# Optimization experiments

Measured on AMD Instinct MI355X. Metric: run time of the kernel, lower is better.

## Reference

```python
import jax, jax.numpy as jnp
import numpy as np

N_HEADS = 16
MAX_CACHE_LEN = 8192
LN_EPS = 1e-5


def _layernorm(x, g, b):
    mu = jnp.mean(x, axis=-1, keepdims=True)
    var = jnp.var(x, axis=-1, keepdims=True)
    return (x - mu) * jax.lax.rsqrt(var + LN_EPS) * g + b


def setup_inputs() -> dict:
    key = jax.random.key(0)
    ks = jax.random.split(key, 8)
    b, t, d, latdim, past = 2, 2048, 2048, 512, 2048
    s = 0.02
    return {
        "x": jax.random.normal(ks[0], (b, t, d), jnp.float32),
        "latent_prev": jax.random.normal(ks[1], (b, past, latdim), jnp.float32),
        "Wq": jax.random.normal(ks[2], (d, d), jnp.float32) * s,
        "Wdown": jax.random.normal(ks[3], (d, latdim), jnp.float32) * s,
        "Wk_up": jax.random.normal(ks[4], (latdim, d), jnp.float32) * s,
        "Wv_up": jax.random.normal(ks[5], (latdim, d), jnp.float32) * s,
        "ln_g": jnp.ones((latdim,), jnp.float32),
        "ln_b": jnp.zeros((latdim,), jnp.float32),
        "Wo": jax.random.normal(ks[6], (d, d), jnp.float32) * s,
    }


def reference(x, latent_prev, Wq, Wdown, Wk_up, Wv_up, ln_g, ln_b, Wo):
    b, t, d = x.shape
    H = N_HEADS
    hd = d // H
    # q projection -> [b, t, H, hd]
    q = (x @ Wq).reshape(b, t, H, hd)
    # latent down-projection + LayerNorm, concat with cache, trim to max_cache_len
    latent_new = _layernorm(x @ Wdown, ln_g, ln_b)
    latent = jnp.concatenate([latent_prev, latent_new], axis=1)
    latent = latent[:, -MAX_CACHE_LEN:]
    S = latent.shape[1]
    past_len = min(latent_prev.shape[1], S - t)
    # up-project K/V from latent -> [b, S, H, hd]
    k = (latent @ Wk_up).reshape(b, S, H, hd)
    v = (latent @ Wv_up).reshape(b, S, H, hd)
    # offset-causal SDPA: query i attends keys j <= past_len + i
    scores = jnp.einsum("bthd,bshd->bhts", q, k) / jnp.sqrt(jnp.asarray(hd, x.dtype))
    i = jnp.arange(t)[:, None]
    j = jnp.arange(S)[None, :]
    mask = j <= (past_len + i)  # [t, S]
    scores = jnp.where(mask[None, None], scores, jnp.asarray(-1e30, scores.dtype))
    attn = jax.nn.softmax(scores, axis=-1)
    out = jnp.einsum("bhts,bshd->bthd", attn, v).reshape(b, t, d)
    return out @ Wo
```

## Files before the change

### kernel.cpp

```cpp
#include <hip/hip_runtime.h>
#include <hip/hip_bf16.h>

using bf16_t = __bf16;
typedef __bf16 bf16x8 __attribute__((ext_vector_type(8)));
typedef __bf16 bf16x4 __attribute__((ext_vector_type(4)));
typedef __bf16 bf16x2 __attribute__((ext_vector_type(2)));
typedef float  f32x4  __attribute__((ext_vector_type(4)));
typedef float  f32x16 __attribute__((ext_vector_type(16)));
typedef unsigned u32x4 __attribute__((ext_vector_type(4)));

#define MFMA16(a,b,c) __builtin_amdgcn_mfma_f32_16x16x32_bf16((a),(b),(c),0,0,0)
#define MFMA32(a,b,c) __builtin_amdgcn_mfma_f32_32x32x16_bf16((a),(b),(c),0,0,0)

__device__ __forceinline__ void load_lds16(const void* g, void* l) {
  __builtin_amdgcn_global_load_lds(
      (const __attribute__((address_space(1))) unsigned int*)g,
      (__attribute__((address_space(3))) unsigned int*)l, 16, 0, 0);
}

__device__ __forceinline__ unsigned pack_bf16(float a, float b) {
  union { bf16x2 v; unsigned u; } c;
  c.v[0] = (bf16_t)a; c.v[1] = (bf16_t)b;
  return c.u;
}

__device__ __forceinline__ float fast_exp2(float x) {
#if __has_builtin(__builtin_amdgcn_exp2f)
  return __builtin_amdgcn_exp2f(x);
#else
  return exp2f(x);
#endif
}

__device__ __forceinline__ void xcd_remap(unsigned& bx, unsigned& by,
                                          unsigned& bz)
{
  const unsigned nxy = gridDim.x * gridDim.y;
  const unsigned nwg = nxy * gridDim.z;
  unsigned wg = (blockIdx.z * gridDim.y + blockIdx.y) * gridDim.x + blockIdx.x;
  if ((nwg & 7u) == 0u)
    wg = (wg & 7u) * (nwg >> 3) + (wg >> 3);
  bz = wg / nxy; wg -= bz * nxy;
  by = wg / gridDim.x;
  bx = wg - by * gridDim.x;
}

__device__ __forceinline__ void transpose_body(const float* __restrict__ in,
                                               bf16_t* __restrict__ out,
                                               int R, int C, int bx, int by,
                                               int tid, bf16_t* t)
{
  const int r0 = by * 64, c0 = bx * 64;
  const int rr = tid >> 4;
  const int c4 = (tid & 15) * 4;
#pragma unroll
  for (int i = 0; i < 4; ++i) {
    const int r = rr + i * 16;
    f32x4 d = *(const f32x4*)(in + (size_t)(r0 + r) * C + c0 + c4);
#pragma unroll
    for (int j = 0; j < 4; ++j) t[(c4 + j) * 80 + r] = (bf16_t)d[j];
  }
  __syncthreads();
  const int a  = tid >> 3;
  const int bc = (tid & 7) * 8;
#pragma unroll
  for (int half = 0; half < 2; ++half) {
    const int cc = a + half * 32;
    bf16x8 d = *(const bf16x8*)&t[cc * 80 + bc];
    *(bf16x8*)(out + (size_t)(c0 + cc) * R + r0 + bc) = d;
  }
}

__global__ __launch_bounds__(256) void prep_all(
    const float* __restrict__ x,     bf16_t* __restrict__ xb,
    const float* __restrict__ Wq,    bf16_t* __restrict__ WqT,
    const float* __restrict__ Wdown, bf16_t* __restrict__ WdT,
    const float* __restrict__ Wo,    bf16_t* __restrict__ WoT,
    const float* __restrict__ Wk,    bf16_t* __restrict__ WkT,
    const float* __restrict__ Wv,    bf16_t* __restrict__ WvT,
    const float* __restrict__ prev,  bf16_t* __restrict__ latent)
{
  __shared__ __align__(16) bf16_t t[64 * 80];
  const int tid = threadIdx.x;
  const unsigned bid = blockIdx.x;
  if (bid < 8192) {
    const size_t i = ((size_t)bid * 256 + tid) * 4;
    f32x4 d = *(const f32x4*)(x + i);
    bf16x4 o;
#pragma unroll
    for (int j = 0; j < 4; ++j) o[j] = (bf16_t)d[j];
    *(bf16x4*)(xb + i) = o;
  } else if (bid < 9216) {
    const unsigned u = bid - 8192;
    transpose_body(Wq, WqT, 2048, 2048, u & 31, u >> 5, tid, t);
  } else if (bid < 9472) {
    const unsigned u = bid - 9216;
    transpose_body(Wdown, WdT, 2048, 512, u & 7, u >> 3, tid, t);
  } else if (bid < 10496) {
    const unsigned u = bid - 9472;
    transpose_body(Wo, WoT, 2048, 2048, u & 31, u >> 5, tid, t);
  } else if (bid < 10752) {
    const unsigned u = bid - 10496;
    transpose_body(Wk, WkT, 512, 2048, u & 31, u >> 5, tid, t);
  } else if (bid < 11008) {
    const unsigned u = bid - 10752;
    transpose_body(Wv, WvT, 512, 2048, u & 31, u >> 5, tid, t);
  } else {
    const size_t v    = (size_t)(bid - 11008) * 256 + tid;
    const size_t flat = v * 4;
    const size_t per  = (size_t)2048 * 512;
    const size_t b    = flat / per, rem = flat % per;
    f32x4 d = *(const f32x4*)(prev + flat);
    bf16x4 o;
#pragma unroll
    for (int j = 0; j < 4; ++j) o[j] = (bf16_t)d[j];
    *(bf16x4*)(latent + b * ((size_t)4096 * 512) + rem) = o;
  }
}

template <typename OutT>
__global__ __launch_bounds__(256) void gemm128(const bf16_t* __restrict__ A,
                                               const bf16_t* __restrict__ BT,
                                               OutT* __restrict__ C,
                                               int M, int N, int K, float scale,
                                               long long zB, long long zC)
{
  __shared__ __align__(16) bf16_t As[128 * 64];
  __shared__ __align__(16) bf16_t Bs[128 * 64];
  const int tid = threadIdx.x;
  unsigned bx, by, bz;
  xcd_remap(bx, by, bz);
  BT += (size_t)bz * zB;
  C  += (size_t)bz * zC;
  const int m0 = by * 128, n0 = bx * 128;
  const int lane = tid & 63, w = tid >> 6;
  const int quad = lane >> 4, l15 = lane & 15;
  const int wm = (w >> 1) * 64, wn = (w & 1) * 64;
  const int s_row = tid >> 3;
  const int g_off = ((tid & 7) ^ (s_row & 7)) * 8;
  const bf16_t* Ap = A  + (size_t)(m0 + s_row) * K + g_off;
  const bf16_t* Bp = BT + (size_t)(n0 + s_row) * K + g_off;
  const int cpos0 = (quad ^ (l15 & 7)) * 8;
  const int cpos1 = ((4 + quad) ^ (l15 & 7)) * 8;

  f32x4 acc[4][4] = {};

  for (int k0 = 0; k0 < K; k0 += 64) {
    __syncthreads();
#pragma unroll
    for (int p = 0; p < 4; ++p) {
      load_lds16(Ap + (size_t)(32 * p) * K + k0, As + (tid + 256 * p) * 8);
      load_lds16(Bp + (size_t)(32 * p) * K + k0, Bs + (tid + 256 * p) * 8);
    }
    __syncthreads();
#pragma unroll
    for (int kk = 0; kk < 2; ++kk) {
      const int cp = kk ? cpos1 : cpos0;
      bf16x8 af[4], bfr[4];
#pragma unroll
      for (int fi = 0; fi < 4; ++fi)
        af[fi] = *(const bf16x8*)&As[(wm + fi * 16 + l15) * 64 + cp];
#pragma unroll
      for (int fj = 0; fj < 4; ++fj)
        bfr[fj] = *(const bf16x8*)&Bs[(wn + fj * 16 + l15) * 64 + cp];
#pragma unroll
      for (int fi = 0; fi < 4; ++fi)
#pragma unroll
        for (int fj = 0; fj < 4; ++fj)
          acc[fi][fj] = MFMA16(af[fi], bfr[fj], acc[fi][fj]);
    }
  }

#pragma unroll
  for (int fi = 0; fi < 4; ++fi)
#pragma unroll
    for (int fj = 0; fj < 4; ++fj)
#pragma unroll
      for (int r = 0; r < 4; ++r) {
        const int row = m0 + wm + fi * 16 + quad * 4 + r;
        const int col = n0 + wn + fj * 16 + l15;
        C[(size_t)row * N + col] = (OutT)(acc[fi][fj][r] * scale);
      }
}

__global__ __launch_bounds__(256) void gemm128_dual(const bf16_t* __restrict__ A,
                                                    const bf16_t* __restrict__ BT,
                                                    bf16_t* __restrict__ C1,
                                                    bf16_t* __restrict__ C2,
                                                    float qscale)
{
  __shared__ __align__(16) bf16_t As[128 * 64];
  __shared__ __align__(16) bf16_t Bs[128 * 64];
  const int tid = threadIdx.x;
  unsigned bx, by, bz;
  xcd_remap(bx, by, bz);
  const int K = 2048;
  const int m0 = by * 128, n0 = bx * 128;
  const int lane = tid & 63, w = tid >> 6;
  const int quad = lane >> 4, l15 = lane & 15;
  const int wm = (w >> 1) * 64, wn = (w & 1) * 64;
  const int s_row = tid >> 3;
  const int g_off = ((tid & 7) ^ (s_row & 7)) * 8;
  const bf16_t* Ap = A  + (size_t)(m0 + s_row) * K + g_off;
  const bf16_t* Bp = BT + (size_t)(n0 + s_row) * K + g_off;
  const int cpos0 = (quad ^ (l15 & 7)) * 8;
  const int cpos1 = ((4 + quad) ^ (l15 & 7)) * 8;

  f32x4 acc[4][4] = {};

  for (int k0 = 0; k0 < K; k0 += 64) {
    __syncthreads();
#pragma unroll
    for (int p = 0; p < 4; ++p) {
      load_lds16(Ap + (size_t)(32 * p) * K + k0, As + (tid + 256 * p) * 8);
      load_lds16(Bp + (size_t)(32 * p) * K + k0, Bs + (tid + 256 * p) * 8);
    }
    __syncthreads();
#pragma unroll
    for (int kk = 0; kk < 2; ++kk) {
      const int cp = kk ? cpos1 : cpos0;
      bf16x8 af[4], bfr[4];
#pragma unroll
      for (int fi = 0; fi < 4; ++fi)
        af[fi] = *(const bf16x8*)&As[(wm + fi * 16 + l15) * 64 + cp];
#pragma unroll
      for (int fj = 0; fj < 4; ++fj)
        bfr[fj] = *(const bf16x8*)&Bs[(wn + fj * 16 + l15) * 64 + cp];
#pragma unroll
      for (int fi = 0; fi < 4; ++fi)
#pragma unroll
        for (int fj = 0; fj < 4; ++fj)
          acc[fi][fj] = MFMA16(af[fi], bfr[fj], acc[fi][fj]);
    }
  }

  const bool isQ = (n0 < 2048);
  const float sc = isQ ? qscale : 1.0f;
#pragma unroll
  for (int fi = 0; fi < 4; ++fi)
#pragma unroll
    for (int fj = 0; fj < 4; ++fj)
#pragma unroll
      for (int r = 0; r < 4; ++r) {
        const int row = m0 + wm + fi * 16 + quad * 4 + r;
        const int col = n0 + wn + fj * 16 + l15;
        if (isQ)
          C1[(size_t)row * 2048 + col] = (bf16_t)(acc[fi][fj][r] * sc);
        else
          C2[(size_t)row * 512 + (col - 2048)] = (bf16_t)(acc[fi][fj][r] * sc);
      }
}

__global__ __launch_bounds__(256) void gemm_kv(const bf16_t* __restrict__ latent,
                                               const bf16_t* __restrict__ WkT,
                                               const bf16_t* __restrict__ WvT,
                                               bf16_t* __restrict__ kbuf,
                                               bf16_t* __restrict__ vTb)
{
  __shared__ __align__(16) bf16_t As[128 * 64];
  __shared__ __align__(16) bf16_t Bs[128 * 64];
  const int tid = threadIdx.x;
  unsigned wg = blockIdx.x;
  wg = (wg & 7u) * 256u + (wg >> 3);
  const bf16_t *A, *BT;
  bf16_t* C;
  int M, N;
  unsigned bx, by;
  if (wg < 1024) {
    bx = wg & 15; by = wg >> 4;
    A = latent; BT = WkT; C = kbuf; M = 8192; N = 2048;
  } else {
    const unsigned t2 = wg - 1024;
    const unsigned bz = t2 >> 9, rem = t2 & 511;
    bx = rem & 31; by = rem >> 5;
    A  = WvT;
    BT = latent + (size_t)bz * ((size_t)4096 * 512);
    C  = vTb + (size_t)bz * ((size_t)2048 * 4096);
    M = 2048; N = 4096;
  }
  const int K = 512;
  const int m0 = by * 128, n0 = bx * 128;
  const int lane = tid & 63, w = tid >> 6;
  const int quad = lane >> 4, l15 = lane & 15;
  const int wm = (w >> 1) * 64, wn = (w & 1) * 64;
  const int s_row = tid >> 3;
  const int g_off = ((tid & 7) ^ (s_row & 7)) * 8;
  const bf16_t* Ap = A  + (size_t)(m0 + s_row) * K + g_off;
  const bf16_t* Bp = BT + (size_t)(n0 + s_row) * K + g_off;
  const int cpos0 = (quad ^ (l15 & 7)) * 8;
  const int cpos1 = ((4 + quad) ^ (l15 & 7)) * 8;

  f32x4 acc[4][4] = {};

  for (int k0 = 0; k0 < K; k0 += 64) {
    __syncthreads();
#pragma unroll
    for (int p = 0; p < 4; ++p) {
      load_lds16(Ap + (size_t)(32 * p) * K + k0, As + (tid + 256 * p) * 8);
      load_lds16(Bp + (size_t)(32 * p) * K + k0, Bs + (tid + 256 * p) * 8);
    }
    __syncthreads();
#pragma unroll
    for (int kk = 0; kk < 2; ++kk) {
      const int cp = kk ? cpos1 : cpos0;
      bf16x8 af[4], bfr[4];
#pragma unroll
      for (int fi = 0; fi < 4; ++fi)
        af[fi] = *(const bf16x8*)&As[(wm + fi * 16 + l15) * 64 + cp];
#pragma unroll
      for (int fj = 0; fj < 4; ++fj)
        bfr[fj] = *(const bf16x8*)&Bs[(wn + fj * 16 + l15) * 64 + cp];
#pragma unroll
      for (int fi = 0; fi < 4; ++fi)
#pragma unroll
        for (int fj = 0; fj < 4; ++fj)
          acc[fi][fj] = MFMA16(af[fi], bfr[fj], acc[fi][fj]);
    }
  }

#pragma unroll
  for (int fi = 0; fi < 4; ++fi)
#pragma unroll
    for (int fj = 0; fj < 4; ++fj)
#pragma unroll
      for (int r = 0; r < 4; ++r) {
        const int row = m0 + wm + fi * 16 + quad * 4 + r;
        const int col = n0 + wn + fj * 16 + l15;
        C[(size_t)row * N + col] = (bf16_t)acc[fi][fj][r];
      }
}

__global__ __launch_bounds__(256) void ln_kernel(const bf16_t* __restrict__ in,
                                                 const float* __restrict__ g_,
                                                 const float* __restrict__ b_,
                                                 bf16_t* __restrict__ latent)
{
  const int row = blockIdx.x;
  const int tid = threadIdx.x;
  const float x0 = (float)in[(size_t)row * 512 + tid];
  const float x1 = (float)in[(size_t)row * 512 + 256 + tid];
  float s  = x0 + x1;
  float sq = x0 * x0 + x1 * x1;
#pragma unroll
  for (int off = 1; off < 64; off <<= 1) {
    s  += __shfl_xor(s, off);
    sq += __shfl_xor(sq, off);
  }
  __shared__ float red[8];
  const int w = tid >> 6;
  if ((tid & 63) == 0) { red[w] = s; red[4 + w] = sq; }
  __syncthreads();
  s  = red[0] + red[1] + red[2] + red[3];
  sq = red[4] + red[5] + red[6] + red[7];
  const float mu   = s * (1.0f / 512.0f);
  const float var  = sq * (1.0f / 512.0f) - mu * mu;
  const float rstd = rsqrtf(var + 1e-5f);
  const int b = row >> 11, tt = row & 2047;
  bf16_t* outp = latent + ((size_t)b * 4096 + 2048 + tt) * 512;
  outp[tid]       = (bf16_t)((x0 - mu) * rstd * g_[tid]       + b_[tid]);
  outp[tid + 256] = (bf16_t)((x1 - mu) * rstd * g_[tid + 256] + b_[tid + 256]);
}

__global__ __launch_bounds__(256) void attn7(const bf16_t* __restrict__ q,
                                             const bf16_t* __restrict__ k,
                                             const bf16_t* __restrict__ vT,
                                             bf16_t* __restrict__ out)
{
  __shared__ __align__(16) bf16_t smem[32768];

  const int tid = threadIdx.x;
  const int lane = tid & 63, w = tid >> 6;
  const int l31 = lane & 31, h5 = lane >> 5;

  const int g = blockIdx.x & 7, j = blockIdx.x >> 3;
  const int jl = j & 31, hsel = j >> 5;
  int qt = jl & 15;
  const int b = jl >> 4;
  if (hsel) qt = 15 - qt;
  const int h = g + 8 * hsel;

  const int q0 = qt * 128;
  const int qg = q0 + l31 * 4 + w;

  bf16x8 qf[8];
  const bf16_t* qb = q + ((size_t)(b * 2048 + qg)) * 2048 + h * 128 + h5 * 8;
#pragma unroll
  for (int fc = 0; fc < 8; ++fc) qf[fc] = *(const bf16x8*)(qb + fc * 16);

  const bf16_t* kbase = k + ((size_t)b * 4096) * 2048 + h * 128;
  const bf16_t* vbase = vT + ((size_t)(b * 16 + h)) * 128 * 4096;

  int ks_key[4], ks_go[4], vs_feat[4], vs_go[4];
#pragma unroll
  for (int p = 0; p < 4; ++p) {
    const int slot = tid + 256 * p;
    const int key = slot >> 4, ph = slot & 15;
    ks_key[p] = key;
    ks_go[p]  = (((ph & 8) | ((ph & 7) ^ (key & 7)))) * 8;
    const int ft = slot >> 3, p2 = slot & 7;
    vs_feat[p] = ft;
    vs_go[p]   = (p2 ^ (ft & 7)) * 8;
  }
  int kfo[8], vfo[4];
#pragma unroll
  for (int fc = 0; fc < 8; ++fc) {
    const int L = fc * 2 + h5;
    kfo[fc] = l31 * 128 + ((L & 8) | ((L & 7) ^ (l31 & 7))) * 8;
  }
#pragma unroll
  for (int kc = 0; kc < 4; ++kc) {
    const int L = kc * 2 + h5;
    vfo[kc] = l31 * 64 + (L ^ (l31 & 7)) * 8;
  }

  f32x16 o[4] = {};
  float m = -1e30f, l = 0.f;
  const int send = 2048 + q0 + 128;

#pragma unroll
  for (int p = 0; p < 4; ++p) {
    load_lds16(kbase + (size_t)ks_key[p] * 2048 + ks_go[p],
               smem + (tid + 256 * p) * 8);
    load_lds16(vbase + (size_t)vs_feat[p] * 4096 + vs_go[p],
               smem + 16384 + (tid + 256 * p) * 8);
  }
  __syncthreads();

  int cur = 0;
  for (int s0 = 0; s0 < send; s0 += 64) {
    const int s1 = s0 + 64;
    if (s1 < send) {
      const int nxt = (cur ^ 1) * 8192;
#pragma unroll
      for (int p = 0; p < 4; ++p) {
        load_lds16(kbase + (size_t)(s1 + ks_key[p]) * 2048 + ks_go[p],
                   smem + nxt + (tid + 256 * p) * 8);
        load_lds16(vbase + (size_t)vs_feat[p] * 4096 + s1 + vs_go[p],
                   smem + 16384 + nxt + (tid + 256 * p) * 8);
      }
    }
    const bf16_t* Kc = smem + cur * 8192;
    const bf16_t* Vc = smem + 16384 + cur * 8192;

    f32x16 st[2] = {};
    __builtin_amdgcn_s_setprio(1);
#pragma unroll
    for (int fc = 0; fc < 8; ++fc) {
      bf16x8 k0 = *(const bf16x8*)&Kc[kfo[fc]];
      bf16x8 k1 = *(const bf16x8*)&Kc[4096 + kfo[fc]];
      st[0] = MFMA32(k0, qf[fc], st[0]);
      st[1] = MFMA32(k1, qf[fc], st[1]);
    }
    __builtin_amdgcn_s_setprio(0);

    if (s0 + 63 > 2048 + q0) {
#pragma unroll
      for (int t = 0; t < 2; ++t)
#pragma unroll
        for (int i = 0; i < 16; ++i) {
          const int key = s0 + 32 * t + (i & 3) + 8 * (i >> 2) + 4 * h5;
          if (key > 2048 + qg) st[t][i] = -1e30f;
        }
    }

    float gm[8];
#pragma unroll
    for (int t = 0; t < 2; ++t)
#pragma unroll
      for (int gg = 0; gg < 4; ++gg)
        gm[t * 4 + gg] = fmaxf(fmaxf(st[t][4 * gg + 0], st[t][4 * gg + 1]),
                               fmaxf(st[t][4 * gg + 2], st[t][4 * gg + 3]));
    float mt = fmaxf(fmaxf(fmaxf(gm[0], gm[1]), fmaxf(gm[2], gm[3])),
                     fmaxf(fmaxf(gm[4], gm[5]), fmaxf(gm[6], gm[7])));
    mt = fmaxf(mt, __shfl_xor(mt, 32));

    if (__any(mt > m + 8.f)) {
      const float mnew = fmaxf(m, mt);
      const float alpha = fast_exp2(m - mnew);
#pragma unroll
      for (int ft = 0; ft < 4; ++ft)
#pragma unroll
        for (int i = 0; i < 16; ++i) o[ft][i] *= alpha;
      l *= alpha;
      m = mnew;
    }

    float rs = 0.f;
    unsigned up[2][4][2];
#pragma unroll
    for (int t = 0; t < 2; ++t)
#pragma unroll
      for (int gg = 0; gg < 4; ++gg) {
        const float p0 = fast_exp2(st[t][4 * gg + 0] - m);
        const float p1 = fast_exp2(st[t][4 * gg + 1] - m);
        const float p2 = fast_exp2(st[t][4 * gg + 2] - m);
        const float p3 = fast_exp2(st[t][4 * gg + 3] - m);
        rs += (p0 + p1) + (p2 + p3);
        up[t][gg][0] = pack_bf16(p0, p1);
        up[t][gg][1] = pack_bf16(p2, p3);
      }
    rs += __shfl_xor(rs, 32);
    l += rs;

#pragma unroll
    for (int kc = 0; kc < 4; ++kc) {
      const int t = kc >> 1, gp = (kc & 1) * 2;
      const unsigned a0 = up[t][gp][0],     a1 = up[t][gp][1];
      const unsigned b0 = up[t][gp + 1][0], b1 = up[t][gp + 1][1];
      const unsigned xa0 = __shfl_xor(a0, 32), xa1 = __shfl_xor(a1, 32);
      const unsigned xb0 = __shfl_xor(b0, 32), xb1 = __shfl_xor(b1, 32);
      u32x4 uw;
      uw[0] = h5 ? xb0 : a0;
      uw[1] = h5 ? xb1 : a1;
      uw[2] = h5 ? b0 : xa0;
      uw[3] = h5 ? b1 : xa1;
      union { u32x4 u; bf16x8 v; } pc; pc.u = uw;
      const bf16x8 pf = pc.v;
      __builtin_amdgcn_s_setprio(1);
#pragma unroll
      for (int ft = 0; ft < 4; ++ft) {
        bf16x8 vf = *(const bf16x8*)&Vc[ft * 2048 + vfo[kc]];
        o[ft] = MFMA32(vf, pf, o[ft]);
      }
      __builtin_amdgcn_s_setprio(0);
    }

    __syncthreads();
    cur ^= 1;
  }

  const float inv = 1.0f / l;
  const int rowp_w = w * 32 + l31;
#pragma unroll
  for (int ft = 0; ft < 4; ++ft)
#pragma unroll
    for (int gg = 0; gg < 4; ++gg) {
      bf16x4 pk;
#pragma unroll
      for (int r = 0; r < 4; ++r) pk[r] = (bf16_t)(o[ft][4 * gg + r] * inv);
      *(bf16x4*)&smem[rowp_w * 136 + ft * 32 + gg * 8 + h5 * 4] = pk;
    }
  __syncthreads();
#pragma unroll
  for (int p = 0; p < 8; ++p) {
    const int c = tid + 256 * p;
    const int rowp = c >> 4, chk = c & 15;
    const int ql = (rowp & 31) * 4 + (rowp >> 5);
    bf16x8 d = *(const bf16x8*)&smem[rowp * 136 + chk * 8];
    *(bf16x8*)(out + ((size_t)(b * 2048 + q0 + ql)) * 2048 + h * 128 + chk * 8) = d;
  }
}

extern "C" void kernel_launch(void* const* d_in, const int* in_sizes, int n_in,
                              void* d_out, int out_size, void* d_ws, size_t ws_size,
                              hipStream_t stream)
{
  (void)in_sizes; (void)n_in; (void)out_size; (void)ws_size;
  const float* x        = (const float*)d_in[0];
  const float* lat_prev = (const float*)d_in[1];
  const float* Wq       = (const float*)d_in[2];
  const float* Wdown    = (const float*)d_in[3];
  const float* Wk_up    = (const float*)d_in[4];
  const float* Wv_up    = (const float*)d_in[5];
  const float* ln_g     = (const float*)d_in[6];
  const float* ln_b     = (const float*)d_in[7];
  const float* Wo       = (const float*)d_in[8];
  float* out = (float*)d_out;

  char* p = (char*)d_ws;
  auto alloc = [&](size_t elems) { bf16_t* r = (bf16_t*)p; p += elems * 2; return r; };
  bf16_t* xb     = alloc((size_t)4096 * 2048);
  bf16_t* WqT    = alloc((size_t)2048 * 2048);
  bf16_t* WdT    = alloc((size_t)512 * 2048);
  bf16_t* qbuf   = alloc((size_t)4096 * 2048);
  bf16_t* latpre = alloc((size_t)4096 * 512);
  bf16_t* latent = alloc((size_t)2 * 4096 * 512);
  bf16_t* kbuf   = alloc((size_t)8192 * 2048);
  bf16_t* vTb    = alloc((size_t)2 * 2048 * 4096);
  bf16_t* aout   = alloc((size_t)4096 * 2048);
  bf16_t* WoT    = alloc((size_t)2048 * 2048);
  bf16_t* WkT    = alloc((size_t)2048 * 512);
  bf16_t* WvT    = alloc((size_t)2048 * 512);

  const dim3 B(256);
  const float qscale = 0.12751744561825988f;

  prep_all<<<dim3(13056), B, 0, stream>>>(x, xb, Wq, WqT, Wdown, WdT,
                                          Wo, WoT, Wk_up, WkT, Wv_up, WvT,
                                          lat_prev, latent);
  gemm128_dual<<<dim3(20, 32), B, 0, stream>>>(xb, WqT, qbuf, latpre, qscale);
  ln_kernel<<<dim3(4096), B, 0, stream>>>(latpre, ln_g, ln_b, latent);
  gemm_kv<<<dim3(2048), B, 0, stream>>>(latent, WkT, WvT, kbuf, vTb);
  attn7<<<dim3(512), B, 0, stream>>>(qbuf, kbuf, vTb, aout);
  gemm128<float><<<dim3(16, 32), B, 0, stream>>>(aout, WoT, out, 4096, 2048, 2048, 1.0f, 0, 0);
}
```

Baseline: 506.8 us.

## Double-buffer LDS in GEMM kernels with 32-wide K tiles

Replaces the single-buffer 64-wide K loop in the three GEMM kernels with a two-stage LDS ping-pong over 32-wide K tiles. The next tile is prefetched with global_load_lds while MFMAs run on the current one, and the swizzle is adapted to 4 chunks per row. This is meant to hide global load latency and remove one barrier per iteration. In exchange each iteration does half the MFMA work, so barrier count per unit of K stays the same. There is also a risk of a race, because the async LDS loads into the other buffer may not be waited on before the single barrier.

Result: no change. 501.8 us (-1.0%).

```diff
diff --git a/kernel.cpp b/kernel.cpp
--- a/kernel.cpp
+++ b/kernel.cpp
@@ -118,6 +118,39 @@
   }
 }
 
+#define GEMM_DBUF_LOOP(Kvar)                                                  \
+  f32x4 acc[4][4] = {};                                                       \
+  auto stage = [&](int k0, int buf) {                                         \
+    bf16_t* Ad = As + buf * 4096;                                             \
+    bf16_t* Bd = Bs + buf * 4096;                                             \
+    load_lds16(Ap0 + k0, Ad + tid * 8);                                       \
+    load_lds16(Ap1 + k0, Ad + tid * 8 + 2048);                                \
+    load_lds16(Bp0 + k0, Bd + tid * 8);                                       \
+    load_lds16(Bp1 + k0, Bd + tid * 8 + 2048);                                \
+  };                                                                          \
+  stage(0, 0);                                                                \
+  __syncthreads();                                                            \
+  int cur = 0;                                                                \
+  for (int k0 = 0; k0 < (Kvar); k0 += 32) {                                   \
+    if (k0 + 32 < (Kvar)) stage(k0 + 32, cur ^ 1);                            \
+    const bf16_t* Ac = As + cur * 4096;                                       \
+    const bf16_t* Bc = Bs + cur * 4096;                                       \
+    bf16x8 af[4], bfr[4];                                                     \
+    _Pragma("unroll")                                                         \
+    for (int fi = 0; fi < 4; ++fi)                                            \
+      af[fi] = *(const bf16x8*)&Ac[(wm + fi * 16 + l15) * 32 + quadp];        \
+    _Pragma("unroll")                                                         \
+    for (int fj = 0; fj < 4; ++fj)                                            \
+      bfr[fj] = *(const bf16x8*)&Bc[(wn + fj * 16 + l15) * 32 + quadp];       \
+    _Pragma("unroll")                                                         \
+    for (int fi = 0; fi < 4; ++fi)                                            \
+      _Pragma("unroll")                                                       \
+      for (int fj = 0; fj < 4; ++fj)                                          \
+        acc[fi][fj] = MFMA16(af[fi], bfr[fj], acc[fi][fj]);                   \
+    __syncthreads();                                                          \
+    cur ^= 1;                                                                 \
+  }
+
 template <typename OutT>
 __global__ __launch_bounds__(256) void gemm128(const bf16_t* __restrict__ A,
                                                const bf16_t* __restrict__ BT,
@@ -125,8 +158,8 @@
                                                int M, int N, int K, float scale,
                                                long long zB, long long zC)
 {
-  __shared__ __align__(16) bf16_t As[128 * 64];
-  __shared__ __align__(16) bf16_t Bs[128 * 64];
+  __shared__ __align__(16) bf16_t As[2 * 128 * 32];
+  __shared__ __align__(16) bf16_t Bs[2 * 128 * 32];
   const int tid = threadIdx.x;
   unsigned bx, by, bz;
   xcd_remap(bx, by, bz);
@@ -136,40 +169,15 @@
   const int lane = tid & 63, w = tid >> 6;
   const int quad = lane >> 4, l15 = lane & 15;
   const int wm = (w >> 1) * 64, wn = (w & 1) * 64;
-  const int s_row = tid >> 3;
-  const int g_off = ((tid & 7) ^ (s_row & 7)) * 8;
-  const bf16_t* Ap = A  + (size_t)(m0 + s_row) * K + g_off;
-  const bf16_t* Bp = BT + (size_t)(n0 + s_row) * K + g_off;
-  const int cpos0 = (quad ^ (l15 & 7)) * 8;
-  const int cpos1 = ((4 + quad) ^ (l15 & 7)) * 8;
-
-  f32x4 acc[4][4] = {};
-
-  for (int k0 = 0; k0 < K; k0 += 64) {
-    __syncthreads();
-#pragma unroll
-    for (int p = 0; p < 4; ++p) {
-      load_lds16(Ap + (size_t)(32 * p) * K + k0, As + (tid + 256 * p) * 8);
-      load_lds16(Bp + (size_t)(32 * p) * K + k0, Bs + (tid + 256 * p) * 8);
-    }
-    __syncthreads();
-#pragma unroll
-    for (int kk = 0; kk < 2; ++kk) {
-      const int cp = kk ? cpos1 : cpos0;
-      bf16x8 af[4], bfr[4];
-#pragma unroll
-      for (int fi = 0; fi < 4; ++fi)
-        af[fi] = *(const bf16x8*)&As[(wm + fi * 16 + l15) * 64 + cp];
-#pragma unroll
-      for (int fj = 0; fj < 4; ++fj)
-        bfr[fj] = *(const bf16x8*)&Bs[(wn + fj * 16 + l15) * 64 + cp];
-#pragma unroll
-      for (int fi = 0; fi < 4; ++fi)
-#pragma unroll
-        for (int fj = 0; fj < 4; ++fj)
-          acc[fi][fj] = MFMA16(af[fi], bfr[fj], acc[fi][fj]);
-    }
-  }
+  const int s_row = tid >> 2;
+  const int g_off = ((tid & 3) ^ (s_row & 3)) * 8;
+  const int quadp = (quad ^ (l15 & 3)) * 8;
+  const bf16_t* Ap0 = A  + (size_t)(m0 + s_row) * K + g_off;
+  const bf16_t* Ap1 = A  + (size_t)(m0 + 64 + s_row) * K + g_off;
+  const bf16_t* Bp0 = BT + (size_t)(n0 + s_row) * K + g_off;
+  const bf16_t* Bp1 = BT + (size_t)(n0 + 64 + s_row) * K + g_off;
+
+  GEMM_DBUF_LOOP(K)
 
 #pragma unroll
   for (int fi = 0; fi < 4; ++fi)
@@ -189,8 +197,8 @@
                                                     bf16_t* __restrict__ C2,
                                                     float qscale)
 {
-  __shared__ __align__(16) bf16_t As[128 * 64];
-  __shared__ __align__(16) bf16_t Bs[128 * 64];
+  __shared__ __align__(16) bf16_t As[2 * 128 * 32];
+  __shared__ __align__(16) bf16_t Bs[2 * 128 * 32];
   const int tid = threadIdx.x;
   unsigned bx, by, bz;
   xcd_remap(bx, by, bz);
@@ -199,40 +207,15 @@
   const int lane = tid & 63, w = tid >> 6;
   const int quad = lane >> 4, l15 = lane & 15;
   const int wm = (w >> 1) * 64, wn = (w & 1) * 64;
-  const int s_row = tid >> 3;
-  const int g_off = ((tid & 7) ^ (s_row & 7)) * 8;
-  const bf16_t* Ap = A  + (size_t)(m0 + s_row) * K + g_off;
-  const bf16_t* Bp = BT + (size_t)(n0 + s_row) * K + g_off;
-  const int cpos0 = (quad ^ (l15 & 7)) * 8;
-  const int cpos1 = ((4 + quad) ^ (l15 & 7)) * 8;
-
-  f32x4 acc[4][4] = {};
-
-  for (int k0 = 0; k0 < K; k0 += 64) {
-    __syncthreads();
-#pragma unroll
-    for (int p = 0; p < 4; ++p) {
-      load_lds16(Ap + (size_t)(32 * p) * K + k0, As + (tid + 256 * p) * 8);
-      load_lds16(Bp + (size_t)(32 * p) * K + k0, Bs + (tid + 256 * p) * 8);
-    }
-    __syncthreads();
-#pragma unroll
-    for (int kk = 0; kk < 2; ++kk) {
-      const int cp = kk ? cpos1 : cpos0;
-      bf16x8 af[4], bfr[4];
-#pragma unroll
-      for (int fi = 0; fi < 4; ++fi)
-        af[fi] = *(const bf16x8*)&As[(wm + fi * 16 + l15) * 64 + cp];
-#pragma unroll
-      for (int fj = 0; fj < 4; ++fj)
-        bfr[fj] = *(const bf16x8*)&Bs[(wn + fj * 16 + l15) * 64 + cp];
-#pragma unroll
-      for (int fi = 0; fi < 4; ++fi)
-#pragma unroll
-        for (int fj = 0; fj < 4; ++fj)
-          acc[fi][fj] = MFMA16(af[fi], bfr[fj], acc[fi][fj]);
-    }
-  }
+  const int s_row = tid >> 2;
+  const int g_off = ((tid & 3) ^ (s_row & 3)) * 8;
+  const int quadp = (quad ^ (l15 & 3)) * 8;
+  const bf16_t* Ap0 = A  + (size_t)(m0 + s_row) * K + g_off;
+  const bf16_t* Ap1 = A  + (size_t)(m0 + 64 + s_row) * K + g_off;
+  const bf16_t* Bp0 = BT + (size_t)(n0 + s_row) * K + g_off;
+  const bf16_t* Bp1 = BT + (size_t)(n0 + 64 + s_row) * K + g_off;
+
+  GEMM_DBUF_LOOP(K)
 
   const bool isQ = (n0 < 2048);
   const float sc = isQ ? qscale : 1.0f;
@@ -257,18 +240,18 @@
                                                bf16_t* __restrict__ kbuf,
                                                bf16_t* __restrict__ vTb)
 {
-  __shared__ __align__(16) bf16_t As[128 * 64];
-  __shared__ __align__(16) bf16_t Bs[128 * 64];
+  __shared__ __align__(16) bf16_t As[2 * 128 * 32];
+  __shared__ __align__(16) bf16_t Bs[2 * 128 * 32];
   const int tid = threadIdx.x;
   unsigned wg = blockIdx.x;
   wg = (wg & 7u) * 256u + (wg >> 3);
   const bf16_t *A, *BT;
   bf16_t* C;
-  int M, N;
+  int N;
   unsigned bx, by;
   if (wg < 1024) {
     bx = wg & 15; by = wg >> 4;
-    A = latent; BT = WkT; C = kbuf; M = 8192; N = 2048;
+    A = latent; BT = WkT; C = kbuf; N = 2048;
   } else {
     const unsigned t2 = wg - 1024;
     const unsigned bz = t2 >> 9, rem = t2 & 511;
@@ -276,47 +259,22 @@
     A  = WvT;
     BT = latent + (size_t)bz * ((size_t)4096 * 512);
     C  = vTb + (size_t)bz * ((size_t)2048 * 4096);
-    M = 2048; N = 4096;
+    N = 4096;
   }
   const int K = 512;
   const int m0 = by * 128, n0 = bx * 128;
   const int lane = tid & 63, w = tid >> 6;
   const int quad = lane >> 4, l15 = lane & 15;
   const int wm = (w >> 1) * 64, wn = (w & 1) * 64;
-  const int s_row = tid >> 3;
-  const int g_off = ((tid & 7) ^ (s_row & 7)) * 8;
-  const bf16_t* Ap = A  + (size_t)(m0 + s_row) * K + g_off;
-  const bf16_t* Bp = BT + (size_t)(n0 + s_row) * K + g_off;
-  const int cpos0 = (quad ^ (l15 & 7)) * 8;
-  const int cpos1 = ((4 + quad) ^ (l15 & 7)) * 8;
-
-  f32x4 acc[4][4] = {};
-
-  for (int k0 = 0; k0 < K; k0 += 64) {
-    __syncthreads();
-#pragma unroll
-    for (int p = 0; p < 4; ++p) {
-      load_lds16(Ap + (size_t)(32 * p) * K + k0, As + (tid + 256 * p) * 8);
-      load_lds16(Bp + (size_t)(32 * p) * K + k0, Bs + (tid + 256 * p) * 8);
-    }
-    __syncthreads();
-#pragma unroll
-    for (int kk = 0; kk < 2; ++kk) {
-      const int cp = kk ? cpos1 : cpos0;
-      bf16x8 af[4], bfr[4];
-#pragma unroll
-      for (int fi = 0; fi < 4; ++fi)
-        af[fi] = *(const bf16x8*)&As[(wm + fi * 16 + l15) * 64 + cp];
-#pragma unroll
-      for (int fj = 0; fj < 4; ++fj)
-        bfr[fj] = *(const bf16x8*)&Bs[(wn + fj * 16 + l15) * 64 + cp];
-#pragma unroll
-      for (int fi = 0; fi < 4; ++fi)
-#pragma unroll
-        for (int fj = 0; fj < 4; ++fj)
-          acc[fi][fj] = MFMA16(af[fi], bfr[fj], acc[fi][fj]);
-    }
-  }
+  const int s_row = tid >> 2;
+  const int g_off = ((tid & 3) ^ (s_row & 3)) * 8;
+  const int quadp = (quad ^ (l15 & 3)) * 8;
+  const bf16_t* Ap0 = A  + (size_t)(m0 + s_row) * K + g_off;
+  const bf16_t* Ap1 = A  + (size_t)(m0 + 64 + s_row) * K + g_off;
+  const bf16_t* Bp0 = BT + (size_t)(n0 + s_row) * K + g_off;
+  const bf16_t* Bp1 = BT + (size_t)(n0 + 64 + s_row) * K + g_off;
+
+  GEMM_DBUF_LOOP(K)
 
 #pragma unroll
   for (int fi = 0; fi < 4; ++fi)
```
